# Performance work log

Measured on AMD Instinct MI355X. Metric: run time of the kernel, lower is better.

## Reference

```python
import jax, jax.numpy as jnp
import numpy as np
from jax import lax

B, T, D, L, OUT, HORIZON, TSLOTS, NDAY = 512, 24, 1024, 2, 325, 12, 288, 7


def setup_inputs() -> dict:
    key = jax.random.key(0)
    ks = jax.random.split(key, 20)
    s_d = 1.0 / np.sqrt(D)
    s_o = 1.0 / np.sqrt(OUT)
    inp = {
        'data': jax.random.normal(ks[0], (B, T, OUT), jnp.float32),
        'time': jax.random.randint(ks[1], (B, T), 0, TSLOTS),
        'weekday': jax.random.randint(ks[2], (B,), 0, NDAY),
        # embedding params
        'w_data': jax.random.normal(ks[3], (OUT, D), jnp.float32) * s_o,
        'b_data': jnp.zeros((D,), jnp.float32),
        'time_table': jax.random.normal(ks[4], (TSLOTS, D), jnp.float32) * 0.02,
        'day_table': jax.random.normal(ks[5], (NDAY, D), jnp.float32) * 0.02,
        # encoder GRU (input_size == hidden_size == D for all layers)
        'enc_Wih': jax.random.uniform(ks[6], (L, 3 * D, D), jnp.float32, -s_d, s_d),
        'enc_Whh': jax.random.uniform(ks[7], (L, 3 * D, D), jnp.float32, -s_d, s_d),
        'enc_bih': jax.random.uniform(ks[8], (L, 3 * D), jnp.float32, -s_d, s_d),
        'enc_bhh': jax.random.uniform(ks[9], (L, 3 * D), jnp.float32, -s_d, s_d),
        # decoder GRU
        'dec_Wih': jax.random.uniform(ks[10], (L, 3 * D, D), jnp.float32, -s_d, s_d),
        'dec_Whh': jax.random.uniform(ks[11], (L, 3 * D, D), jnp.float32, -s_d, s_d),
        'dec_bih': jax.random.uniform(ks[12], (L, 3 * D), jnp.float32, -s_d, s_d),
        'dec_bhh': jax.random.uniform(ks[13], (L, 3 * D), jnp.float32, -s_d, s_d),
        # decoder output MLP (dropout=0 -> linear)
        'w_mlp': jax.random.uniform(ks[14], (D, OUT), jnp.float32, -s_d, s_d),
        'b_mlp': jnp.zeros((OUT,), jnp.float32),
    }
    return inp


def _gru_cell(h, x, Wih, Whh, bih, bhh):
    # torch GRUCell math. h,x: [B,D]
    gx = x @ Wih.T + bih            # [B,3D]
    gh = h @ Whh.T + bhh
    xr, xz, xn = jnp.split(gx, 3, axis=-1)
    hr, hz, hn = jnp.split(gh, 3, axis=-1)
    r = jax.nn.sigmoid(xr + hr)
    z = jax.nn.sigmoid(xz + hz)
    n = jnp.tanh(xn + r * hn)
    return (1.0 - z) * n + z * h


def _gru_layer(x, h0, Wih, Whh, bih, bhh):
    # x: [B,S,D] -> outputs [B,S,D], final h [B,D]
    def step(h, xt):
        h2 = _gru_cell(h, xt, Wih, Whh, bih, bhh)
        return h2, h2
    hT, ys = lax.scan(step, h0, jnp.moveaxis(x, 1, 0))
    return jnp.moveaxis(ys, 0, 1), hT


def reference(data, time, weekday, w_data, b_data, time_table, day_table,
              enc_Wih, enc_Whh, enc_bih, enc_bhh,
              dec_Wih, dec_Whh, dec_bih, dec_bhh, w_mlp, b_mlp):
    def embed(d, t, wd):  # d:[B,S,OUT] t:[B,S] wd:[B]
        return (d @ w_data + b_data
                + time_table[t % TSLOTS]
                + day_table[wd][:, None, :])

    # ---- encoder over history (all but last step) ----
    x = embed(data[:, :-1], time[:, :-1], weekday)  # [B,T-1,D]
    h_layers = []
    for l in range(L):
        x, hl = _gru_layer(x, jnp.zeros((B, D), x.dtype),
                           enc_Wih[l], enc_Whh[l], enc_bih[l], enc_bhh[l])
        h_layers.append(hl)
    hidden = jnp.stack(h_layers)  # [L,B,D]

    def dec_step(carry, _):
        hidden, data_i, time_i = carry  # [L,B,D], [B,1,OUT], [B,1]
        xi = embed(data_i, time_i, weekday)[:, 0]  # [B,D]
        new_h = []
        h_in = xi
        for l in range(L):
            hl = _gru_cell(hidden[l], h_in, dec_Wih[l], dec_Whh[l],
                           dec_bih[l], dec_bhh[l])
            new_h.append(hl)
            h_in = hl
        res = h_in @ w_mlp + b_mlp              # [B,OUT]
        out_i = data_i[:, 0] + res
        data_next = data_i[:, 0] + lax.stop_gradient(res)
        return (jnp.stack(new_h), data_next[:, None], time_i + 1), out_i

    carry0 = (hidden, data[:, -1:], time[:, -1:])
    _, outs = lax.scan(dec_step, carry0, None, length=HORIZON)  # [H,B,OUT]
    return jnp.moveaxis(outs, 0, 1)  # [B,H,OUT]
```

## Files before the change

### kernel.cpp

```cpp
#include <hip/hip_runtime.h>
#include <math.h>

#define B_ 512
#define T_ 24
#define TM1 23
#define D_ 1024
#define OUT_ 325
#define HORIZON_ 12

typedef unsigned short ushort_t;
typedef __attribute__((ext_vector_type(8))) short bf16x8;
typedef __attribute__((ext_vector_type(4))) float f32x4;

#define MFMA16(a, b, c) __builtin_amdgcn_mfma_f32_16x16x32_bf16((a), (b), (c), 0, 0, 0)

__device__ __forceinline__ ushort_t f2b(float f) {
  union { float f; unsigned u; } v; v.f = f;
  unsigned r = (v.u + 0x7fffu + ((v.u >> 16) & 1u)) >> 16;
  return (ushort_t)r;
}
__device__ __forceinline__ float b2f(ushort_t s) {
  union { unsigned u; float f; } v; v.u = ((unsigned)s) << 16;
  return v.f;
}

__device__ __forceinline__ size_t pidx16(int m, int k, int K) {
  return (((size_t)(m >> 4) * (K >> 5) + (k >> 5)) * 64
          + ((m & 15) + (((k >> 3) & 3) << 4))) * 8 + (k & 7);
}

#define GLOAD16(src, dst) \
  __builtin_amdgcn_global_load_lds((const __attribute__((address_space(1))) void*)(src), \
                                   (__attribute__((address_space(3))) void*)(dst), 16, 0, 0)

__global__ __launch_bounds__(256) void enc_diag(
    int k,
    const ushort_t* __restrict__ Hp0, const float* __restrict__ Hf0,
    float* __restrict__ Hf0o, ushort_t* __restrict__ Hp0o,
    const ushort_t* __restrict__ Whh0, const float* __restrict__ bhh0,
    const ushort_t* __restrict__ GXbuf, ushort_t* __restrict__ Y0p,
    const ushort_t* __restrict__ Wih1, const float* __restrict__ bih1,
    ushort_t* __restrict__ GX1p,
    const ushort_t* __restrict__ Hp1, const float* __restrict__ Hf1,
    float* __restrict__ Hf1o, ushort_t* __restrict__ Hp1o,
    const ushort_t* __restrict__ Whh1, const float* __restrict__ bhh1)
{
  __shared__ ushort_t lds[2][8 * 512];
  const int tid = threadIdx.x, lane = tid & 63, w = tid >> 6;
  const int bid = blockIdx.x;
  const int z = bid >> 9, bx = (bid >> 5) & 15, by = bid & 31;
  const int wm = w >> 1, wn = w & 1;
  const int d = by * 32 + wn * 16 + (lane & 15);

  const ushort_t *Abase, *Bbase;
  if (z == 0) {
    if (k >= TM1) return;
    Abase = Hp0; Bbase = Whh0;
  } else if (z == 1) {
    if (k < 1 || k > TM1) return;
    Abase = Y0p + (size_t)(k - 1) * 512 * 1024; Bbase = Wih1;
  } else {
    if (k < 2) return;
    Abase = Hp1; Bbase = Whh1;
  }

  f32x4 acc[3] = {};
  auto stage = [&](int buf, int kb) {
    #pragma unroll
    for (int r = 0; r < 2; ++r) {
      int s = w * 2 + r;
      const ushort_t* src;
      if (s < 2) src = Abase + ((size_t)(((bx * 32 + s * 16) >> 4) * 32 + kb)) * 512 + lane * 8;
      else { int g = (s - 2) >> 1, hf = (s - 2) & 1;
        src = Bbase + ((size_t)((g * 64 + by * 2 + hf) * 32 + kb)) * 512 + lane * 8; }
      GLOAD16(src, &lds[buf][s * 512 + lane * 8]);
    }
  };
  stage(0, 0); __syncthreads();
  int cur = 0;
  for (int kb = 0; kb < 32; ++kb) {
    if (kb + 1 < 32) stage(cur ^ 1, kb + 1);
    const ushort_t* L = lds[cur];
    bf16x8 a = *(const bf16x8*)(L + wm * 512 + lane * 8);
    #pragma unroll
    for (int g = 0; g < 3; ++g) {
      bf16x8 b = *(const bf16x8*)(L + (2 + g * 2 + wn) * 512 + lane * 8);
      acc[g] = MFMA16(a, b, acc[g]);
    }
    __syncthreads(); cur ^= 1;
  }

  if (z == 1) {
    ushort_t* G = GX1p + (size_t)((k - 1) & 1) * 512 * 3072;
    #pragma unroll
    for (int q = 0; q < 4; ++q) {
      int m = bx * 32 + wm * 16 + ((lane >> 4) << 2) + q;
      #pragma unroll
      for (int g = 0; g < 3; ++g) {
        int n = g * 1024 + d;
        G[pidx16(m, n, 3072)] = f2b(acc[g][q] + bih1[n]);
      }
    }
    return;
  }

  const float* bhh = (z == 0) ? bhh0 : bhh1;
  const float* Hf  = (z == 0) ? Hf0 : Hf1;
  float* HfO       = (z == 0) ? Hf0o : Hf1o;
  ushort_t* HpO    = (z == 0) ? Hp0o : Hp1o;
  const float bh_r = bhh[d], bh_z = bhh[D_ + d], bh_n = bhh[2 * D_ + d];
  const ushort_t* GXrow = (z == 0) ? (GXbuf + (size_t)k * 512 * 3072) : nullptr;
  const ushort_t* G2 = (z == 2) ? (GX1p + (size_t)(k & 1) * 512 * 3072) : nullptr;
  ushort_t* Seqp = (z == 0) ? (Y0p + (size_t)k * 512 * 1024) : nullptr;
  #pragma unroll
  for (int q = 0; q < 4; ++q) {
    int m = bx * 32 + wm * 16 + ((lane >> 4) << 2) + q;
    float gx_r, gx_z, gx_n;
    if (z == 0) {
      const ushort_t* gxp = GXrow + (size_t)m * 3072 + d;
      gx_r = b2f(gxp[0]); gx_z = b2f(gxp[D_]); gx_n = b2f(gxp[2 * D_]);
    } else {
      gx_r = b2f(G2[pidx16(m, d, 3072)]);
      gx_z = b2f(G2[pidx16(m, D_ + d, 3072)]);
      gx_n = b2f(G2[pidx16(m, 2 * D_ + d, 3072)]);
    }
    float rr = 1.f / (1.f + __expf(-(gx_r + acc[0][q] + bh_r)));
    float zz = 1.f / (1.f + __expf(-(gx_z + acc[1][q] + bh_z)));
    float nn = tanhf(gx_n + rr * (acc[2][q] + bh_n));
    float h = Hf[(size_t)m * D_ + d];
    float hnew = (1.f - zz) * nn + zz * h;
    HfO[(size_t)m * D_ + d] = hnew;
    ushort_t hb = f2b(hnew);
    size_t pi = pidx16(m, d, D_);
    HpO[pi] = hb;
    if (z == 0) Seqp[pi] = hb;
  }
}

__global__ __launch_bounds__(256) void dec_cell0(
    const ushort_t* __restrict__ DCp, const ushort_t* __restrict__ Hp,
    const float* __restrict__ Hf,
    const ushort_t* __restrict__ W0dp, const ushort_t* __restrict__ Whh0,
    const float* __restrict__ bhh0,
    const float* __restrict__ CTt, const float* __restrict__ CBd,
    const int* __restrict__ timev, int step,
    float* __restrict__ Hf_out, ushort_t* __restrict__ Hp_out)
{
  __shared__ ushort_t lds[2][16 * 512];
  const int tid = threadIdx.x, lane = tid & 63, w = tid >> 6;
  const int bid = blockIdx.x;
  const int bx = bid >> 5, by = bid & 31;
  const int wm = w >> 1, wn = w & 1;
  const int d = by * 32 + wn * 16 + (lane & 15);
  f32x4 accx[3] = {}, acch[3] = {};

  auto stage_h = [&](int buf, int kb) {
    #pragma unroll
    for (int r = 0; r < 2; ++r) {
      int s = (w == 0) ? (2 + r) : (8 + w * 2 + r);
      const ushort_t* src;
      if (s < 4) src = Hp + ((size_t)(((bx * 32 + (s - 2) * 16) >> 4) * 32 + kb)) * 512 + lane * 8;
      else { int g = (s - 10) >> 1, hf = (s - 10) & 1;
        src = Whh0 + ((size_t)((g * 64 + by * 2 + hf) * 32 + kb)) * 512 + lane * 8; }
      GLOAD16(src, &lds[buf][s * 512 + lane * 8]);
    }
  };
  auto stage_x = [&](int buf, int kb) {
    #pragma unroll
    for (int r = 0; r < 2; ++r) {
      int s = (w == 0) ? r : (2 + w * 2 + r);
      const ushort_t* src;
      if (s < 2) src = DCp + ((size_t)(((bx * 32 + s * 16) >> 4) * 11 + kb)) * 512 + lane * 8;
      else { int g = (s - 4) >> 1, hf = (s - 4) & 1;
        src = W0dp + ((size_t)((g * 64 + by * 2 + hf) * 11 + kb)) * 512 + lane * 8; }
      GLOAD16(src, &lds[buf][s * 512 + lane * 8]);
    }
  };

  stage_h(0, 0); stage_x(0, 0);
  __syncthreads();
  int cur = 0;
  for (int kb = 0; kb < 32; ++kb) {
    if (kb + 1 < 32) {
      stage_h(cur ^ 1, kb + 1);
      if (kb + 1 < 11) stage_x(cur ^ 1, kb + 1);
    }
    const ushort_t* L = lds[cur];
    bf16x8 ah = *(const bf16x8*)(L + (2 + wm) * 512 + lane * 8);
    if (kb < 11) {
      bf16x8 ax = *(const bf16x8*)(L + (0 + wm) * 512 + lane * 8);
      #pragma unroll
      for (int g = 0; g < 3; ++g) {
        bf16x8 bxw = *(const bf16x8*)(L + (4 + g * 2 + wn) * 512 + lane * 8);
        accx[g] = MFMA16(ax, bxw, accx[g]);
      }
    }
    #pragma unroll
    for (int g = 0; g < 3; ++g) {
      bf16x8 bhw = *(const bf16x8*)(L + (10 + g * 2 + wn) * 512 + lane * 8);
      acch[g] = MFMA16(ah, bhw, acch[g]);
    }
    __syncthreads(); cur ^= 1;
  }

  const float bh_r = bhh0[d], bh_z = bhh0[D_ + d], bh_n = bhh0[2 * D_ + d];
  #pragma unroll
  for (int q = 0; q < 4; ++q) {
    int m = bx * 32 + wm * 16 + ((lane >> 4) << 2) + q;
    int ti = (timev[m * T_ + (T_ - 1)] + step) % 288;
    const float* ctt = CTt + (size_t)ti * 3072;
    const float* cb  = CBd + (size_t)m * 3072;
    float gx_r = accx[0][q] + ctt[d] + cb[d];
    float gx_z = accx[1][q] + ctt[D_ + d] + cb[D_ + d];
    float gx_n = accx[2][q] + ctt[2 * D_ + d] + cb[2 * D_ + d];
    float rr = 1.f / (1.f + __expf(-(gx_r + acch[0][q] + bh_r)));
    float zz = 1.f / (1.f + __expf(-(gx_z + acch[1][q] + bh_z)));
    float nn = tanhf(gx_n + rr * (acch[2][q] + bh_n));
    float h = Hf[(size_t)m * D_ + d];
    float hnew = (1.f - zz) * nn + zz * h;
    Hf_out[(size_t)m * D_ + d] = hnew;
    Hp_out[pidx16(m, d, D_)] = f2b(hnew);
  }
}

__global__ __launch_bounds__(256) void gru_cell32(
    const ushort_t* __restrict__ Xp_, const ushort_t* __restrict__ Hp,
    const float* __restrict__ Hf,
    const ushort_t* __restrict__ Wih_l, const ushort_t* __restrict__ Whh_l,
    const float* __restrict__ bih_l, const float* __restrict__ bhh_l,
    float* __restrict__ Hf_out, ushort_t* __restrict__ Hp_out)
{
  __shared__ ushort_t lds[2][16 * 512];
  const int tid = threadIdx.x, lane = tid & 63, w = tid >> 6;
  const int bid = blockIdx.x;
  const int bx = bid >> 5, by = bid & 31;
  const int wm = w >> 1, wn = w & 1;
  const int d = by * 32 + wn * 16 + (lane & 15);
  f32x4 accx[3] = {}, acch[3] = {};

  auto stage = [&](int buf, int kb) {
    #pragma unroll
    for (int r = 0; r < 4; ++r) {
      int s = w * 4 + r;
      const ushort_t* src;
      if (s < 2) src = Xp_ + ((size_t)(((bx * 32 + s * 16) >> 4) * 32 + kb)) * 512 + lane * 8;
      else if (s < 4) src = Hp + ((size_t)(((bx * 32 + (s - 2) * 16) >> 4) * 32 + kb)) * 512 + lane * 8;
      else if (s < 10) { int g = (s - 4) >> 1, hf = (s - 4) & 1;
        src = Wih_l + ((size_t)((g * 64 + by * 2 + hf) * 32 + kb)) * 512 + lane * 8; }
      else { int g = (s - 10) >> 1, hf = (s - 10) & 1;
        src = Whh_l + ((size_t)((g * 64 + by * 2 + hf) * 32 + kb)) * 512 + lane * 8; }
      GLOAD16(src, &lds[buf][s * 512 + lane * 8]);
    }
  };

  stage(0, 0); __syncthreads();
  int cur = 0;
  for (int kb = 0; kb < 32; ++kb) {
    if (kb + 1 < 32) stage(cur ^ 1, kb + 1);
    const ushort_t* L = lds[cur];
    bf16x8 ax = *(const bf16x8*)(L + (0 + wm) * 512 + lane * 8);
    bf16x8 ah = *(const bf16x8*)(L + (2 + wm) * 512 + lane * 8);
    #pragma unroll
    for (int g = 0; g < 3; ++g) {
      bf16x8 bxw = *(const bf16x8*)(L + (4 + g * 2 + wn) * 512 + lane * 8);
      bf16x8 bhw = *(const bf16x8*)(L + (10 + g * 2 + wn) * 512 + lane * 8);
      accx[g] = MFMA16(ax, bxw, accx[g]);
      acch[g] = MFMA16(ah, bhw, acch[g]);
    }
    __syncthreads(); cur ^= 1;
  }

  const float bi_r = bih_l[d], bi_z = bih_l[D_ + d], bi_n = bih_l[2 * D_ + d];
  const float bh_r = bhh_l[d], bh_z = bhh_l[D_ + d], bh_n = bhh_l[2 * D_ + d];
  #pragma unroll
  for (int q = 0; q < 4; ++q) {
    int m = bx * 32 + wm * 16 + ((lane >> 4) << 2) + q;
    float rr = 1.f / (1.f + __expf(-(accx[0][q] + bi_r + acch[0][q] + bh_r)));
    float zz = 1.f / (1.f + __expf(-(accx[1][q] + bi_z + acch[1][q] + bh_z)));
    float nn = tanhf(accx[2][q] + bi_n + rr * (acch[2][q] + bh_n));
    float h = Hf[(size_t)m * D_ + d];
    float hnew = (1.f - zz) * nn + zz * h;
    Hf_out[(size_t)m * D_ + d] = hnew;
    Hp_out[pidx16(m, d, D_)] = f2b(hnew);
  }
}

__global__ __launch_bounds__(256) void gemm_gx0_enc(
    const ushort_t* __restrict__ Ap, const ushort_t* __restrict__ W0p,
    const float* __restrict__ CTt, const float* __restrict__ CBe,
    const int* __restrict__ timev,
    ushort_t* __restrict__ GX)
{
  __shared__ ushort_t lds[2][16 * 512];
  const int tid = threadIdx.x, lane = tid & 63, w = tid >> 6;
  const int bx = blockIdx.x, by = blockIdx.y;
  const int wm = w >> 1, wn = w & 1;
  f32x4 acc[4][4] = {};

  auto stage = [&](int buf, int kb) {
    #pragma unroll
    for (int r = 0; r < 4; ++r) {
      int s = r * 4 + w;
      const ushort_t* src = (s < 8)
          ? Ap  + ((size_t)((bx * 8 + s) * 11 + kb)) * 512 + lane * 8
          : W0p + ((size_t)((by * 8 + (s - 8)) * 11 + kb)) * 512 + lane * 8;
      GLOAD16(src, &lds[buf][s * 512 + lane * 8]);
    }
  };

  stage(0, 0); __syncthreads();
  int cur = 0;
  for (int kb = 0; kb < 11; ++kb) {
    if (kb + 1 < 11) stage(cur ^ 1, kb + 1);
    const ushort_t* L = lds[cur];
    bf16x8 af[4], bf[4];
    #pragma unroll
    for (int f = 0; f < 4; ++f) {
      af[f] = *(const bf16x8*)(L + (wm * 4 + f) * 512 + lane * 8);
      bf[f] = *(const bf16x8*)(L + (8 + wn * 4 + f) * 512 + lane * 8);
    }
    #pragma unroll
    for (int fm = 0; fm < 4; ++fm)
      #pragma unroll
      for (int fn = 0; fn < 4; ++fn)
        acc[fm][fn] = MFMA16(af[fm], bf[fn], acc[fm][fn]);
    __syncthreads(); cur ^= 1;
  }

  float* fl = (float*)&lds[0][0];
  for (int fm = 0; fm < 4; ++fm) {
    #pragma unroll
    for (int q = 0; q < 4; ++q)
      #pragma unroll
      for (int fn = 0; fn < 4; ++fn)
        fl[(wm * 16 + ((lane >> 4) << 2) + q) * 132 + wn * 64 + fn * 16 + (lane & 15)]
            = acc[fm][fn][q];
    __syncthreads();
    #pragma unroll
    for (int it = 0; it < 2; ++it) {
      int idx = it * 256 + tid;
      int ml = idx >> 4, n0 = (idx & 15) * 8;
      int m = bx * 128 + (ml >> 4) * 64 + fm * 16 + (ml & 15);
      int b = m / 23, t = m - b * 23;
      int ti = timev[b * T_ + t] % 288;
      const float* ctt = CTt + (size_t)ti * 3072 + by * 128 + n0;
      const float* cb  = CBe + (size_t)b * 3072 + by * 128 + n0;
      const float* fr  = fl + ml * 132 + n0;
      bf16x8 o;
      #pragma unroll
      for (int j = 0; j < 8; ++j) o[j] = f2b(fr[j] + ctt[j] + cb[j]);
      *(bf16x8*)(GX + ((size_t)t * 512 + b) * 3072 + by * 128 + n0) = o;
    }
    __syncthreads();
  }
}

template<int EPI>
__global__ __launch_bounds__(256) void gemm64(
    const ushort_t* __restrict__ Ap, const ushort_t* __restrict__ Wp, int K32,
    const float* __restrict__ bias, int step,
    ushort_t* __restrict__ outp, float* __restrict__ outf,
    float* __restrict__ dout, ushort_t* __restrict__ DCp)
{
  __shared__ ushort_t lds[2][8 * 512];
  const int tid = threadIdx.x, lane = tid & 63, w = tid >> 6;
  const int bx = blockIdx.x, by = blockIdx.y;
  const int wm = w >> 1, wn = w & 1;
  f32x4 acc[2][2] = {};

  auto stage = [&](int buf, int kb) {
    #pragma unroll
    for (int r = 0; r < 2; ++r) {
      int s = r * 4 + w;
      const ushort_t* src = (s < 4)
          ? Ap + ((size_t)((bx * 4 + s) * K32 + kb)) * 512 + lane * 8
          : Wp + ((size_t)((by * 4 + (s - 4)) * K32 + kb)) * 512 + lane * 8;
      GLOAD16(src, &lds[buf][s * 512 + lane * 8]);
    }
  };

  stage(0, 0); __syncthreads();
  int cur = 0;
  for (int kb = 0; kb < K32; ++kb) {
    if (kb + 1 < K32) stage(cur ^ 1, kb + 1);
    const ushort_t* L = lds[cur];
    bf16x8 af[2], bf[2];
    #pragma unroll
    for (int f = 0; f < 2; ++f) {
      af[f] = *(const bf16x8*)(L + (wm * 2 + f) * 512 + lane * 8);
      bf[f] = *(const bf16x8*)(L + (4 + wn * 2 + f) * 512 + lane * 8);
    }
    #pragma unroll
    for (int fm = 0; fm < 2; ++fm)
      #pragma unroll
      for (int fn = 0; fn < 2; ++fn)
        acc[fm][fn] = MFMA16(af[fm], bf[fn], acc[fm][fn]);
    __syncthreads(); cur ^= 1;
  }

  #pragma unroll
  for (int fm = 0; fm < 2; ++fm) {
    #pragma unroll
    for (int q = 0; q < 4; ++q) {
      int m = bx * 64 + wm * 32 + fm * 16 + ((lane >> 4) << 2) + q;
      #pragma unroll
      for (int fn = 0; fn < 2; ++fn) {
        int n = by * 64 + wn * 32 + fn * 16 + (lane & 15);
        float v = acc[fm][fn][q];
        if (EPI == 0) {
          if (n < 352) outp[pidx16(m, n, 352)] = f2b(v);
        } else if (EPI == 1) {
          outf[(size_t)m * 3072 + n] = v;
        } else {
          if (n < OUT_) {
            v += bias[n] + outf[(size_t)m * OUT_ + n];
            dout[((size_t)m * HORIZON_ + step) * OUT_ + n] = v;
            outf[(size_t)m * OUT_ + n] = v;
            DCp[pidx16(m, n, 352)] = f2b(v);
          }
        }
      }
    }
  }
}

__global__ void build_cb(const float* __restrict__ CT, const float* __restrict__ bih0,
                         const int* __restrict__ weekday, float* __restrict__ CB)
{
  int idx = blockIdx.x * 256 + threadIdx.x;
  if (idx >= 512 * 3072) return;
  int b = idx / 3072, n = idx - b * 3072;
  CB[idx] = CT[(size_t)(288 + weekday[b]) * 3072 + n] + CT[(size_t)295 * 3072 + n] + bih0[n];
}

__global__ void pack_k1024(const float* __restrict__ src, ushort_t* __restrict__ dst,
                           int total, int Mvalid) {
  int stride = gridDim.x * 256;
  for (int i = blockIdx.x * 256 + threadIdx.x; i < total; i += stride) {
    int seg = i >> 6, q = i & 63;
    int m = (seg >> 5) * 16 + (q & 15);
    int k = (seg & 31) * 32 + (q >> 4) * 8;
    bf16x8 o;
    if (m < Mvalid) {
      const float* s = src + (size_t)m * 1024 + k;
      float4 v0 = *(const float4*)s, v1 = *(const float4*)(s + 4);
      o[0] = f2b(v0.x); o[1] = f2b(v0.y); o[2] = f2b(v0.z); o[3] = f2b(v0.w);
      o[4] = f2b(v1.x); o[5] = f2b(v1.y); o[6] = f2b(v1.z); o[7] = f2b(v1.w);
    } else o = bf16x8{0,0,0,0,0,0,0,0};
    *(bf16x8*)(dst + (size_t)i * 8) = o;
  }
}
__global__ void pack_wm(const float* __restrict__ w_mlp, ushort_t* __restrict__ dst) {
  int stride = gridDim.x * 256;
  for (int i = blockIdx.x * 256 + threadIdx.x; i < 384 * 128; i += stride) {
    int seg = i >> 6, q = i & 63;
    int n = (seg >> 5) * 16 + (q & 15);
    int k = (seg & 31) * 32 + (q >> 4) * 8;
    bf16x8 o;
    #pragma unroll
    for (int j = 0; j < 8; ++j)
      o[j] = (n < OUT_) ? f2b(w_mlp[(size_t)(k + j) * OUT_ + n]) : (short)0;
    *(bf16x8*)(dst + (size_t)i * 8) = o;
  }
}
__global__ void pack_ct(const float* __restrict__ time_table, const float* __restrict__ day_table,
                        const float* __restrict__ b_data, ushort_t* __restrict__ dst) {
  int stride = gridDim.x * 256;
  for (int i = blockIdx.x * 256 + threadIdx.x; i < 320 * 128; i += stride) {
    int seg = i >> 6, q = i & 63;
    int r = (seg >> 5) * 16 + (q & 15);
    int k = (seg & 31) * 32 + (q >> 4) * 8;
    const float* s = nullptr;
    if (r < 288) s = time_table + (size_t)r * 1024 + k;
    else if (r < 295) s = day_table + (size_t)(r - 288) * 1024 + k;
    else if (r == 295) s = b_data + k;
    bf16x8 o;
    #pragma unroll
    for (int j = 0; j < 8; ++j) o[j] = s ? f2b(s[j]) : (short)0;
    *(bf16x8*)(dst + (size_t)i * 8) = o;
  }
}
__global__ void pack_ae(const float* __restrict__ data, ushort_t* __restrict__ Ap) {
  int stride = gridDim.x * 256;
  const int total = (11776 / 16) * 11 * 64;
  for (int i = blockIdx.x * 256 + threadIdx.x; i < total; i += stride) {
    int seg = i >> 6, q = i & 63;
    int m = (seg / 11) * 16 + (q & 15);
    int k = (seg % 11) * 32 + (q >> 4) * 8;
    int b = m / TM1, t = m - b * TM1;
    const float* s = data + ((size_t)b * T_ + t) * OUT_;
    bf16x8 o;
    #pragma unroll
    for (int j = 0; j < 8; ++j) {
      int kk = k + j;
      o[j] = (kk < OUT_) ? f2b(s[kk]) : (short)0;
    }
    *(bf16x8*)(Ap + (size_t)i * 8) = o;
  }
}
__global__ void pack_dc(const float* __restrict__ data, ushort_t* __restrict__ DCp,
                        float* __restrict__ DC) {
  int stride = gridDim.x * 256;
  const int total = (512 / 16) * 11 * 64;
  for (int i = blockIdx.x * 256 + threadIdx.x; i < total; i += stride) {
    int seg = i >> 6, q = i & 63;
    int b = (seg / 11) * 16 + (q & 15);
    int k = (seg % 11) * 32 + (q >> 4) * 8;
    const float* s = data + ((size_t)b * T_ + (T_ - 1)) * OUT_;
    bf16x8 o;
    #pragma unroll
    for (int j = 0; j < 8; ++j) {
      int kk = k + j;
      float v = (kk < OUT_) ? s[kk] : 0.f;
      o[j] = f2b(v);
      if (kk < OUT_) DC[(size_t)b * OUT_ + kk] = v;
    }
    *(bf16x8*)(DCp + (size_t)i * 8) = o;
  }
}

extern "C" void kernel_launch(void* const* d_in, const int* in_sizes, int n_in,
                              void* d_out, int out_size, void* d_ws, size_t ws_size,
                              hipStream_t stream) {
  const float* data       = (const float*)d_in[0];
  const int*   timev      = (const int*)  d_in[1];
  const int*   weekday    = (const int*)  d_in[2];
  const float* w_data     = (const float*)d_in[3];
  const float* b_data     = (const float*)d_in[4];
  const float* time_table = (const float*)d_in[5];
  const float* day_table  = (const float*)d_in[6];
  const float* enc_Wih    = (const float*)d_in[7];
  const float* enc_Whh    = (const float*)d_in[8];
  const float* enc_bih    = (const float*)d_in[9];
  const float* enc_bhh    = (const float*)d_in[10];
  const float* dec_Wih    = (const float*)d_in[11];
  const float* dec_Whh    = (const float*)d_in[12];
  const float* dec_bih    = (const float*)d_in[13];
  const float* dec_bhh    = (const float*)d_in[14];
  const float* w_mlp      = (const float*)d_in[15];
  const float* b_mlp      = (const float*)d_in[16];
  float* out = (float*)d_out;

  char* base = (char*)d_ws;
  size_t o = 0;
  auto take = [&](size_t bytes) { void* p = base + o; o = (o + bytes + 511) & ~(size_t)511; return p; };
  const size_t WSZ = (size_t)6144 * 1024 * 2;
  ushort_t* Wih_e = (ushort_t*)take(WSZ);
  ushort_t* Whh_e = (ushort_t*)take(WSZ);
  ushort_t* Wih_d = (ushort_t*)take(WSZ);
  ushort_t* Whh_d = (ushort_t*)take(WSZ);
  ushort_t* WdTk  = (ushort_t*)take((size_t)384 * 1024 * 2);
  ushort_t* WmT   = (ushort_t*)take((size_t)384 * 1024 * 2);
  ushort_t* CTpk  = (ushort_t*)take((size_t)320 * 1024 * 2);
  ushort_t* W0ep  = (ushort_t*)take((size_t)3072 * 352 * 2);
  ushort_t* W0dp  = (ushort_t*)take((size_t)3072 * 352 * 2);
  float*    CTe   = (float*)take((size_t)320 * 3072 * 4);
  float*    CTd   = (float*)take((size_t)320 * 3072 * 4);
  float*    CBe   = (float*)take((size_t)512 * 3072 * 4);
  float*    CBd   = (float*)take((size_t)512 * 3072 * 4);
  ushort_t* Ap    = (ushort_t*)take((size_t)11776 * 352 * 2);
  ushort_t* Xp    = (ushort_t*)take((size_t)23 * 512 * 1024 * 2);
  ushort_t* GXbuf = (ushort_t*)take((size_t)23 * 512 * 3072 * 2);
  ushort_t* GX1p  = (ushort_t*)take((size_t)2 * 512 * 3072 * 2);
  ushort_t* DCp   = (ushort_t*)take((size_t)512 * 352 * 2);
  float*    DC    = (float*)take((size_t)512 * OUT_ * 4);
  float*    Hfb   = (float*)take((size_t)4 * 512 * 1024 * 4 + (size_t)4 * 512 * 1024 * 2);
  if (o > ws_size) return;

  float* Hf0[2], *Hf1[2]; ushort_t* Hp0[2], *Hp1[2];
  ushort_t* Hpb = (ushort_t*)(Hfb + (size_t)4 * 512 * 1024);
  for (int p = 0; p < 2; ++p) {
    Hf0[p] = Hfb + (size_t)p * 512 * 1024;
    Hf1[p] = Hfb + (size_t)(2 + p) * 512 * 1024;
    Hp0[p] = Hpb + (size_t)p * 512 * 1024;
    Hp1[p] = Hpb + (size_t)(2 + p) * 512 * 1024;
  }

  const size_t WLAYER = (size_t)3072 * 1024;

  pack_k1024<<<3072, 256, 0, stream>>>(enc_Wih, Wih_e, 6144 * 128, 6144);
  pack_k1024<<<3072, 256, 0, stream>>>(enc_Whh, Whh_e, 6144 * 128, 6144);
  pack_k1024<<<3072, 256, 0, stream>>>(dec_Wih, Wih_d, 6144 * 128, 6144);
  pack_k1024<<<3072, 256, 0, stream>>>(dec_Whh, Whh_d, 6144 * 128, 6144);
  pack_k1024<<<192, 256, 0, stream>>>(w_data, WdTk, 384 * 128, OUT_);
  pack_wm<<<192, 256, 0, stream>>>(w_mlp, WmT);
  pack_ct<<<160, 256, 0, stream>>>(time_table, day_table, b_data, CTpk);
  pack_ae<<<2048, 256, 0, stream>>>(data, Ap);
  pack_dc<<<88, 256, 0, stream>>>(data, DCp, DC);

  gemm64<0><<<dim3(48, 6), 256, 0, stream>>>(Wih_e, WdTk, 32, nullptr, 0, W0ep, nullptr, nullptr, nullptr);
  gemm64<0><<<dim3(48, 6), 256, 0, stream>>>(Wih_d, WdTk, 32, nullptr, 0, W0dp, nullptr, nullptr, nullptr);
  gemm64<1><<<dim3(5, 48), 256, 0, stream>>>(CTpk, Wih_e, 32, nullptr, 0, nullptr, CTe, nullptr, nullptr);
  gemm64<1><<<dim3(5, 48), 256, 0, stream>>>(CTpk, Wih_d, 32, nullptr, 0, nullptr, CTd, nullptr, nullptr);
  build_cb<<<6144, 256, 0, stream>>>(CTe, enc_bih, weekday, CBe);
  build_cb<<<6144, 256, 0, stream>>>(CTd, dec_bih, weekday, CBd);

  gemm_gx0_enc<<<dim3(92, 24), 256, 0, stream>>>(Ap, W0ep, CTe, CBe, timev, GXbuf);

  hipMemsetAsync(Hf0[0], 0, (size_t)512 * 1024 * 4, stream);
  hipMemsetAsync(Hf1[0], 0, (size_t)512 * 1024 * 4, stream);
  hipMemsetAsync(Hp0[0], 0, (size_t)512 * 1024 * 2, stream);
  hipMemsetAsync(Hp1[0], 0, (size_t)512 * 1024 * 2, stream);

  int p0 = 0, p1 = 0;
  for (int k = 0; k <= TM1 + 1; ++k) {
    enc_diag<<<1536, 256, 0, stream>>>(k,
        Hp0[p0], Hf0[p0], Hf0[1 - p0], Hp0[1 - p0], Whh_e, enc_bhh, GXbuf, Xp,
        Wih_e + WLAYER, enc_bih + 3072, GX1p,
        Hp1[p1], Hf1[p1], Hf1[1 - p1], Hp1[1 - p1],
        Whh_e + WLAYER, enc_bhh + 3072);
    if (k < TM1) p0 ^= 1;
    if (k >= 2)  p1 ^= 1;
  }

  for (int s = 0; s < HORIZON_; ++s) {
    dec_cell0<<<512, 256, 0, stream>>>(
        DCp, Hp0[p0], Hf0[p0], W0dp, Whh_d, dec_bhh, CTd, CBd, timev, s,
        Hf0[1 - p0], Hp0[1 - p0]);
    p0 ^= 1;
    gru_cell32<<<512, 256, 0, stream>>>(
        Hp0[p0], Hp1[p1], Hf1[p1],
        Wih_d + WLAYER, Whh_d + WLAYER, dec_bih + 3072, dec_bhh + 3072,
        Hf1[1 - p1], Hp1[1 - p1]);
    p1 ^= 1;
    gemm64<3><<<dim3(8, 6), 256, 0, stream>>>(
        Hp1[p1], WmT, 32, b_mlp, s, nullptr, DC, out, DCp);
  }
}
```

Baseline: 1.405 ms.

## Double M-tile per block in encoder diagonal kernel and store GX in batch-major order

Each enc_diag block now computes a 64-row M tile with two MFMA accumulators per gate, so each staged weight tile is reused across twice as many rows, and the grid shrinks from 1536 to 768 blocks. The precomputed layer-0 input gates are written as row m = b*23+t instead of t-major, and the encoder reads them with the matching index. This cuts weight traffic from L2/LDS per step, at the cost of fewer blocks, lower occupancy, and a strided GX read pattern in the encoder.

```diff
diff --git a/kernel.cpp b/kernel.cpp
--- a/kernel.cpp
+++ b/kernel.cpp
@@ -45,10 +45,10 @@
     float* __restrict__ Hf1o, ushort_t* __restrict__ Hp1o,
     const ushort_t* __restrict__ Whh1, const float* __restrict__ bhh1)
 {
-  __shared__ ushort_t lds[2][8 * 512];
+  __shared__ ushort_t lds[2][10 * 512];
   const int tid = threadIdx.x, lane = tid & 63, w = tid >> 6;
   const int bid = blockIdx.x;
-  const int z = bid >> 9, bx = (bid >> 5) & 15, by = bid & 31;
+  const int z = bid >> 8, bx = (bid >> 5) & 7, by = bid & 31;
   const int wm = w >> 1, wn = w & 1;
   const int d = by * 32 + wn * 16 + (lane & 15);
 
@@ -64,14 +64,15 @@
     Abase = Hp1; Bbase = Whh1;
   }
 
-  f32x4 acc[3] = {};
+  f32x4 acc[3][2] = {};
   auto stage = [&](int buf, int kb) {
     #pragma unroll
-    for (int r = 0; r < 2; ++r) {
-      int s = w * 2 + r;
+    for (int r = 0; r < 3; ++r) {
+      int s = r * 4 + w;
+      if (s >= 10) break;
       const ushort_t* src;
-      if (s < 2) src = Abase + ((size_t)(((bx * 32 + s * 16) >> 4) * 32 + kb)) * 512 + lane * 8;
-      else { int g = (s - 2) >> 1, hf = (s - 2) & 1;
+      if (s < 4) src = Abase + ((size_t)((bx * 4 + s) * 32 + kb)) * 512 + lane * 8;
+      else { int g = (s - 4) >> 1, hf = (s - 4) & 1;
         src = Bbase + ((size_t)((g * 64 + by * 2 + hf) * 32 + kb)) * 512 + lane * 8; }
       GLOAD16(src, &lds[buf][s * 512 + lane * 8]);
     }
@@ -81,11 +82,13 @@
   for (int kb = 0; kb < 32; ++kb) {
     if (kb + 1 < 32) stage(cur ^ 1, kb + 1);
     const ushort_t* L = lds[cur];
-    bf16x8 a = *(const bf16x8*)(L + wm * 512 + lane * 8);
+    bf16x8 a0 = *(const bf16x8*)(L + (wm * 2 + 0) * 512 + lane * 8);
+    bf16x8 a1 = *(const bf16x8*)(L + (wm * 2 + 1) * 512 + lane * 8);
     #pragma unroll
     for (int g = 0; g < 3; ++g) {
-      bf16x8 b = *(const bf16x8*)(L + (2 + g * 2 + wn) * 512 + lane * 8);
-      acc[g] = MFMA16(a, b, acc[g]);
+      bf16x8 b = *(const bf16x8*)(L + (4 + g * 2 + wn) * 512 + lane * 8);
+      acc[g][0] = MFMA16(a0, b, acc[g][0]);
+      acc[g][1] = MFMA16(a1, b, acc[g][1]);
     }
     __syncthreads(); cur ^= 1;
   }
@@ -93,12 +96,15 @@
   if (z == 1) {
     ushort_t* G = GX1p + (size_t)((k - 1) & 1) * 512 * 3072;
     #pragma unroll
-    for (int q = 0; q < 4; ++q) {
-      int m = bx * 32 + wm * 16 + ((lane >> 4) << 2) + q;
+    for (int fm = 0; fm < 2; ++fm) {
       #pragma unroll
-      for (int g = 0; g < 3; ++g) {
-        int n = g * 1024 + d;
-        G[pidx16(m, n, 3072)] = f2b(acc[g][q] + bih1[n]);
+      for (int q = 0; q < 4; ++q) {
+        int m = bx * 64 + wm * 32 + fm * 16 + ((lane >> 4) << 2) + q;
+        #pragma unroll
+        for (int g = 0; g < 3; ++g) {
+          int n = g * 1024 + d;
+          G[pidx16(m, n, 3072)] = f2b(acc[g][fm][q] + bih1[n]);
+        }
       }
     }
     return;
@@ -109,31 +115,33 @@
   float* HfO       = (z == 0) ? Hf0o : Hf1o;
   ushort_t* HpO    = (z == 0) ? Hp0o : Hp1o;
   const float bh_r = bhh[d], bh_z = bhh[D_ + d], bh_n = bhh[2 * D_ + d];
-  const ushort_t* GXrow = (z == 0) ? (GXbuf + (size_t)k * 512 * 3072) : nullptr;
   const ushort_t* G2 = (z == 2) ? (GX1p + (size_t)(k & 1) * 512 * 3072) : nullptr;
   ushort_t* Seqp = (z == 0) ? (Y0p + (size_t)k * 512 * 1024) : nullptr;
   #pragma unroll
-  for (int q = 0; q < 4; ++q) {
-    int m = bx * 32 + wm * 16 + ((lane >> 4) << 2) + q;
-    float gx_r, gx_z, gx_n;
-    if (z == 0) {
-      const ushort_t* gxp = GXrow + (size_t)m * 3072 + d;
-      gx_r = b2f(gxp[0]); gx_z = b2f(gxp[D_]); gx_n = b2f(gxp[2 * D_]);
-    } else {
-      gx_r = b2f(G2[pidx16(m, d, 3072)]);
-      gx_z = b2f(G2[pidx16(m, D_ + d, 3072)]);
-      gx_n = b2f(G2[pidx16(m, 2 * D_ + d, 3072)]);
-    }
-    float rr = 1.f / (1.f + __expf(-(gx_r + acc[0][q] + bh_r)));
-    float zz = 1.f / (1.f + __expf(-(gx_z + acc[1][q] + bh_z)));
-    float nn = tanhf(gx_n + rr * (acc[2][q] + bh_n));
-    float h = Hf[(size_t)m * D_ + d];
-    float hnew = (1.f - zz) * nn + zz * h;
-    HfO[(size_t)m * D_ + d] = hnew;
-    ushort_t hb = f2b(hnew);
-    size_t pi = pidx16(m, d, D_);
-    HpO[pi] = hb;
-    if (z == 0) Seqp[pi] = hb;
+  for (int fm = 0; fm < 2; ++fm) {
+    #pragma unroll
+    for (int q = 0; q < 4; ++q) {
+      int m = bx * 64 + wm * 32 + fm * 16 + ((lane >> 4) << 2) + q;
+      float gx_r, gx_z, gx_n;
+      if (z == 0) {
+        const ushort_t* gxp = GXbuf + (size_t)(m * 23 + k) * 3072 + d;
+        gx_r = b2f(gxp[0]); gx_z = b2f(gxp[D_]); gx_n = b2f(gxp[2 * D_]);
+      } else {
+        gx_r = b2f(G2[pidx16(m, d, 3072)]);
+        gx_z = b2f(G2[pidx16(m, D_ + d, 3072)]);
+        gx_n = b2f(G2[pidx16(m, 2 * D_ + d, 3072)]);
+      }
+      float rr = 1.f / (1.f + __expf(-(gx_r + acc[0][fm][q] + bh_r)));
+      float zz = 1.f / (1.f + __expf(-(gx_z + acc[1][fm][q] + bh_z)));
+      float nn = tanhf(gx_n + rr * (acc[2][fm][q] + bh_n));
+      float h = Hf[(size_t)m * D_ + d];
+      float hnew = (1.f - zz) * nn + zz * h;
+      HfO[(size_t)m * D_ + d] = hnew;
+      ushort_t hb = f2b(hnew);
+      size_t pi = pidx16(m, d, D_);
+      HpO[pi] = hb;
+      if (z == 0) Seqp[pi] = hb;
+    }
   }
 }
 
@@ -349,7 +357,7 @@
       bf16x8 o;
       #pragma unroll
       for (int j = 0; j < 8; ++j) o[j] = f2b(fr[j] + ctt[j] + cb[j]);
-      *(bf16x8*)(GX + ((size_t)t * 512 + b) * 3072 + by * 128 + n0) = o;
+      *(bf16x8*)(GX + (size_t)m * 3072 + by * 128 + n0) = o;
     }
     __syncthreads();
   }
@@ -604,7 +612,7 @@
 
   int p0 = 0, p1 = 0;
   for (int k = 0; k <= TM1 + 1; ++k) {
-    enc_diag<<<1536, 256, 0, stream>>>(k,
+    enc_diag<<<768, 256, 0, stream>>>(k,
         Hp0[p0], Hf0[p0], Hf0[1 - p0], Hp0[1 - p0], Whh_e, enc_bhh, GXbuf, Xp,
         Wih_e + WLAYER, enc_bih + 3072, GX1p,
         Hp1[p1], Hf1[p1], Hf1[1 - p1], Hp1[1 - p1],
```

Measured after the change: 1.514 ms. +7.7%, slower.

## Stage two K-blocks per barrier in GRU kernels and coalesce pack reads

Applied to the files above, without the earlier changes.

The encoder-diagonal and GRU cell kernels now load two 32-wide K blocks per pipeline stage, doubling the LDS buffers. This halves the number of loop iterations and __syncthreads barriers. Separately, pack_k1024 and pack_ae change which thread reads which (m,k) element so that consecutive threads read contiguous fp32 addresses, while the packed output layout stays the same. The trade-off is double the LDS per block, which can lower occupancy.

```diff
diff --git a/kernel.cpp b/kernel.cpp
--- a/kernel.cpp
+++ b/kernel.cpp
@@ -45,7 +45,7 @@
     float* __restrict__ Hf1o, ushort_t* __restrict__ Hp1o,
     const ushort_t* __restrict__ Whh1, const float* __restrict__ bhh1)
 {
-  __shared__ ushort_t lds[2][8 * 512];
+  __shared__ ushort_t lds[2][16 * 512];
   const int tid = threadIdx.x, lane = tid & 63, w = tid >> 6;
   const int bid = blockIdx.x;
   const int z = bid >> 9, bx = (bid >> 5) & 15, by = bid & 31;
@@ -65,27 +65,32 @@
   }
 
   f32x4 acc[3] = {};
-  auto stage = [&](int buf, int kb) {
-    #pragma unroll
-    for (int r = 0; r < 2; ++r) {
-      int s = w * 2 + r;
+  auto stage = [&](int buf, int kb2) {
+    #pragma unroll
+    for (int r = 0; r < 4; ++r) {
+      int s = r * 4 + w;
+      int half = s >> 3, s8 = s & 7;
+      int kb = kb2 * 2 + half;
       const ushort_t* src;
-      if (s < 2) src = Abase + ((size_t)(((bx * 32 + s * 16) >> 4) * 32 + kb)) * 512 + lane * 8;
-      else { int g = (s - 2) >> 1, hf = (s - 2) & 1;
+      if (s8 < 2) src = Abase + ((size_t)(((bx * 32 + s8 * 16) >> 4) * 32 + kb)) * 512 + lane * 8;
+      else { int g = (s8 - 2) >> 1, hf = (s8 - 2) & 1;
         src = Bbase + ((size_t)((g * 64 + by * 2 + hf) * 32 + kb)) * 512 + lane * 8; }
       GLOAD16(src, &lds[buf][s * 512 + lane * 8]);
     }
   };
   stage(0, 0); __syncthreads();
   int cur = 0;
-  for (int kb = 0; kb < 32; ++kb) {
-    if (kb + 1 < 32) stage(cur ^ 1, kb + 1);
-    const ushort_t* L = lds[cur];
-    bf16x8 a = *(const bf16x8*)(L + wm * 512 + lane * 8);
-    #pragma unroll
-    for (int g = 0; g < 3; ++g) {
-      bf16x8 b = *(const bf16x8*)(L + (2 + g * 2 + wn) * 512 + lane * 8);
-      acc[g] = MFMA16(a, b, acc[g]);
+  for (int kb2 = 0; kb2 < 16; ++kb2) {
+    if (kb2 + 1 < 16) stage(cur ^ 1, kb2 + 1);
+    #pragma unroll
+    for (int half = 0; half < 2; ++half) {
+      const ushort_t* Lh = &lds[cur][half * 8 * 512];
+      bf16x8 a = *(const bf16x8*)(Lh + wm * 512 + lane * 8);
+      #pragma unroll
+      for (int g = 0; g < 3; ++g) {
+        bf16x8 b = *(const bf16x8*)(Lh + (2 + g * 2 + wn) * 512 + lane * 8);
+        acc[g] = MFMA16(a, b, acc[g]);
+      }
     }
     __syncthreads(); cur ^= 1;
   }
@@ -230,7 +235,7 @@
     const float* __restrict__ bih_l, const float* __restrict__ bhh_l,
     float* __restrict__ Hf_out, ushort_t* __restrict__ Hp_out)
 {
-  __shared__ ushort_t lds[2][16 * 512];
+  __shared__ ushort_t lds[2][32 * 512];
   const int tid = threadIdx.x, lane = tid & 63, w = tid >> 6;
   const int bid = blockIdx.x;
   const int bx = bid >> 5, by = bid & 31;
@@ -238,16 +243,18 @@
   const int d = by * 32 + wn * 16 + (lane & 15);
   f32x4 accx[3] = {}, acch[3] = {};
 
-  auto stage = [&](int buf, int kb) {
-    #pragma unroll
-    for (int r = 0; r < 4; ++r) {
-      int s = w * 4 + r;
+  auto stage = [&](int buf, int kb2) {
+    #pragma unroll
+    for (int r = 0; r < 8; ++r) {
+      int s = r * 4 + w;
+      int half = s >> 4, s16 = s & 15;
+      int kb = kb2 * 2 + half;
       const ushort_t* src;
-      if (s < 2) src = Xp_ + ((size_t)(((bx * 32 + s * 16) >> 4) * 32 + kb)) * 512 + lane * 8;
-      else if (s < 4) src = Hp + ((size_t)(((bx * 32 + (s - 2) * 16) >> 4) * 32 + kb)) * 512 + lane * 8;
-      else if (s < 10) { int g = (s - 4) >> 1, hf = (s - 4) & 1;
+      if (s16 < 2) src = Xp_ + ((size_t)(((bx * 32 + s16 * 16) >> 4) * 32 + kb)) * 512 + lane * 8;
+      else if (s16 < 4) src = Hp + ((size_t)(((bx * 32 + (s16 - 2) * 16) >> 4) * 32 + kb)) * 512 + lane * 8;
+      else if (s16 < 10) { int g = (s16 - 4) >> 1, hf = (s16 - 4) & 1;
         src = Wih_l + ((size_t)((g * 64 + by * 2 + hf) * 32 + kb)) * 512 + lane * 8; }
-      else { int g = (s - 10) >> 1, hf = (s - 10) & 1;
+      else { int g = (s16 - 10) >> 1, hf = (s16 - 10) & 1;
         src = Whh_l + ((size_t)((g * 64 + by * 2 + hf) * 32 + kb)) * 512 + lane * 8; }
       GLOAD16(src, &lds[buf][s * 512 + lane * 8]);
     }
@@ -255,17 +262,20 @@
 
   stage(0, 0); __syncthreads();
   int cur = 0;
-  for (int kb = 0; kb < 32; ++kb) {
-    if (kb + 1 < 32) stage(cur ^ 1, kb + 1);
-    const ushort_t* L = lds[cur];
-    bf16x8 ax = *(const bf16x8*)(L + (0 + wm) * 512 + lane * 8);
-    bf16x8 ah = *(const bf16x8*)(L + (2 + wm) * 512 + lane * 8);
-    #pragma unroll
-    for (int g = 0; g < 3; ++g) {
-      bf16x8 bxw = *(const bf16x8*)(L + (4 + g * 2 + wn) * 512 + lane * 8);
-      bf16x8 bhw = *(const bf16x8*)(L + (10 + g * 2 + wn) * 512 + lane * 8);
-      accx[g] = MFMA16(ax, bxw, accx[g]);
-      acch[g] = MFMA16(ah, bhw, acch[g]);
+  for (int kb2 = 0; kb2 < 16; ++kb2) {
+    if (kb2 + 1 < 16) stage(cur ^ 1, kb2 + 1);
+    #pragma unroll
+    for (int half = 0; half < 2; ++half) {
+      const ushort_t* Lh = &lds[cur][half * 16 * 512];
+      bf16x8 ax = *(const bf16x8*)(Lh + (0 + wm) * 512 + lane * 8);
+      bf16x8 ah = *(const bf16x8*)(Lh + (2 + wm) * 512 + lane * 8);
+      #pragma unroll
+      for (int g = 0; g < 3; ++g) {
+        bf16x8 bxw = *(const bf16x8*)(Lh + (4 + g * 2 + wn) * 512 + lane * 8);
+        bf16x8 bhw = *(const bf16x8*)(Lh + (10 + g * 2 + wn) * 512 + lane * 8);
+        accx[g] = MFMA16(ax, bxw, accx[g]);
+        acch[g] = MFMA16(ah, bhw, acch[g]);
+      }
     }
     __syncthreads(); cur ^= 1;
   }
@@ -438,8 +448,8 @@
   int stride = gridDim.x * 256;
   for (int i = blockIdx.x * 256 + threadIdx.x; i < total; i += stride) {
     int seg = i >> 6, q = i & 63;
-    int m = (seg >> 5) * 16 + (q & 15);
-    int k = (seg & 31) * 32 + (q >> 4) * 8;
+    int m = (seg >> 5) * 16 + (q >> 2);
+    int k = (seg & 31) * 32 + (q & 3) * 8;
     bf16x8 o;
     if (m < Mvalid) {
       const float* s = src + (size_t)m * 1024 + k;
@@ -447,7 +457,7 @@
       o[0] = f2b(v0.x); o[1] = f2b(v0.y); o[2] = f2b(v0.z); o[3] = f2b(v0.w);
       o[4] = f2b(v1.x); o[5] = f2b(v1.y); o[6] = f2b(v1.z); o[7] = f2b(v1.w);
     } else o = bf16x8{0,0,0,0,0,0,0,0};
-    *(bf16x8*)(dst + (size_t)i * 8) = o;
+    *(bf16x8*)(dst + ((size_t)seg * 64 + (q >> 2) + (q & 3) * 16) * 8) = o;
   }
 }
 __global__ void pack_wm(const float* __restrict__ w_mlp, ushort_t* __restrict__ dst) {
@@ -485,8 +495,8 @@
   const int total = (11776 / 16) * 11 * 64;
   for (int i = blockIdx.x * 256 + threadIdx.x; i < total; i += stride) {
     int seg = i >> 6, q = i & 63;
-    int m = (seg / 11) * 16 + (q & 15);
-    int k = (seg % 11) * 32 + (q >> 4) * 8;
+    int m = (seg / 11) * 16 + (q >> 2);
+    int k = (seg % 11) * 32 + (q & 3) * 8;
     int b = m / TM1, t = m - b * TM1;
     const float* s = data + ((size_t)b * T_ + t) * OUT_;
     bf16x8 o;
@@ -495,7 +505,7 @@
       int kk = k + j;
       o[j] = (kk < OUT_) ? f2b(s[kk]) : (short)0;
     }
-    *(bf16x8*)(Ap + (size_t)i * 8) = o;
+    *(bf16x8*)(Ap + ((size_t)seg * 64 + (q >> 2) + (q & 3) * 16) * 8) = o;
   }
 }
 __global__ void pack_dc(const float* __restrict__ data, ushort_t* __restrict__ DCp,
```

Measured after the change: 1.408 ms (median of 2 runs). No clear change (+0.2%).
